# Kernel tuning notes

Measured on AMD Instinct MI355X. Metric: run time of the kernel, lower is better.

## Reference

```python
import jax, jax.numpy as jnp
import numpy as np

E, B, S, C, N, D, DFF, H, K_FREQ = 4, 16, 256, 17, 16, 32, 64, 4, 4
DH = D // H
MA_KERNELS = (4, 8, 12)


def setup_inputs() -> dict:
    key = jax.random.key(0)
    ks = jax.random.split(key, 16)
    sc = 1.0 / np.sqrt(D).astype(np.float32)
    inp = {
        "x": jax.random.normal(ks[0], (B, S, C, 1), jnp.float32),
        "original_x": jax.random.uniform(ks[1], (B, S, 2), jnp.float32),
        "start_W": jax.random.normal(ks[2], (D,), jnp.float32),
        "start_b": jnp.zeros((D,), jnp.float32),
        "Wq": jax.random.normal(ks[3], (E, D, D), jnp.float32) * sc,
        "Wk": jax.random.normal(ks[4], (E, D, D), jnp.float32) * sc,
        "Wv": jax.random.normal(ks[5], (E, D, D), jnp.float32) * sc,
        "Wo": jax.random.normal(ks[6], (E, D, D), jnp.float32) * sc,
        "ln1_g": jnp.ones((E, D), jnp.float32),
        "ln1_b": jnp.zeros((E, D), jnp.float32),
        "ln2_g": jnp.ones((E, D), jnp.float32),
        "ln2_b": jnp.zeros((E, D), jnp.float32),
        "W1": jax.random.normal(ks[7], (E, D, DFF), jnp.float32) * sc,
        "b1": jnp.zeros((E, DFF), jnp.float32),
        "W2": jax.random.normal(ks[8], (E, DFF, D), jnp.float32) * (1.0 / np.sqrt(DFF).astype(np.float32)),
        "b2": jnp.zeros((E, D), jnp.float32),
    }
    return inp


def _moving_avg(x, k):
    # x: [B,S,Ch], replicate-pad then uniform window of size k (stride 1)
    front = jnp.repeat(x[:, :1], (k - 1) // 2, axis=1)
    end = jnp.repeat(x[:, -1:], k // 2, axis=1)
    xp = jnp.concatenate([front, x, end], axis=1)  # [B, S+k-1, Ch]
    c = jnp.cumsum(xp, axis=1)
    c = jnp.concatenate([jnp.zeros_like(c[:, :1]), c], axis=1)
    return (c[:, k:] - c[:, :-k]) / jnp.asarray(k, x.dtype)


def _fourier_season(x, k):
    # ETSformer-style FourierLayer: keep top-k amplitude frequencies (excluding DC)
    s = x.shape[1]
    xf = jnp.fft.rfft(x, axis=1)            # [B,F,Ch] complex
    amp = jnp.abs(xf)
    amp = amp.at[:, 0, :].set(-jnp.inf)     # exclude DC
    topv = jax.lax.top_k(jnp.moveaxis(amp, 1, -1), k)[0]  # [B,Ch,k]
    thresh = topv[..., -1]                  # [B,Ch]
    mask = amp >= thresh[:, None, :]
    xf_m = jnp.where(mask, xf, 0)
    return jnp.fft.irfft(xf_m, n=s, axis=1).astype(x.dtype)


def _ln(z, g, b):
    m = jnp.mean(z, -1, keepdims=True)
    v = jnp.var(z, -1, keepdims=True)
    return (z - m) * jax.lax.rsqrt(v + 1e-5) * g + b


def _expert_fwd(args):
    h, wq, wk, wv, wo, g1, bg1, g2, bg2, w1, b1e, w2, b2e = args
    # h: [B,S,N,D]; pre-LN MHA over the sequence axis per (batch, node)
    z = _ln(h, g1, bg1)
    q = jnp.einsum('bsnd,de->bsne', z, wq).reshape(B, S, N, H, DH)
    k_ = jnp.einsum('bsnd,de->bsne', z, wk).reshape(B, S, N, H, DH)
    v_ = jnp.einsum('bsnd,de->bsne', z, wv).reshape(B, S, N, H, DH)
    att = jnp.einsum('bqnhd,bknhd->bnhqk', q, k_) * (1.0 / np.sqrt(DH).astype(np.float32))
    att = jax.nn.softmax(att, axis=-1)
    o = jnp.einsum('bnhqk,bknhd->bqnhd', att, v_).reshape(B, S, N, D)
    h = h + jnp.einsum('bsnd,de->bsne', o, wo)
    z2 = _ln(h, g2, bg2)
    f = jax.nn.relu(jnp.einsum('bsnd,df->bsnf', z2, w1) + b1e)
    h = h + jnp.einsum('bsnf,fd->bsnd', f, w2) + b2e
    return h


def reference(x, original_x, start_W, start_b, Wq, Wk, Wv, Wo,
              ln1_g, ln1_b, ln2_g, ln2_b, W1, b1, W2, b2):
    xc = x[:, :, :, 0]                                  # [B,S,C]
    trend = sum(_moving_avg(xc, k) for k in MA_KERNELS) / float(len(MA_KERNELS))
    season = _fourier_season(xc, K_FREQ)
    new_x = xc + season + trend                         # [B,S,C]

    scores = original_x[:, :, -1]                       # [B,S]
    bins = jnp.linspace(scores.min(), scores.max(), E + 1)
    assign = jnp.clip(jnp.searchsorted(bins, scores, side='right') - 1, 0, E - 1)  # [B,S] int

    xns = new_x[:, :, :-1]                              # [B,S,N] drop score channel
    onehot = (assign[None] == jnp.arange(E)[:, None, None])          # [E,B,S] bool
    expert_in = xns[None] * onehot[..., None].astype(xns.dtype)      # [E,B,S,N] dense zero-padded dispatch
    hidden = expert_in[..., None] * start_W + start_b                # [E,B,S,N,D] start_linear

    outs = jax.lax.map(_expert_fwd, (hidden, Wq, Wk, Wv, Wo,
                                     ln1_g, ln1_b, ln2_g, ln2_b, W1, b1, W2, b2))  # [E,B,S,N,D]
    combined = jnp.einsum('ebs,ebsnd->bsnd', onehot.astype(outs.dtype), outs)      # one-hot combine
    return combined
```

## Files before the change

kernel.cpp:

```cpp
#include <hip/hip_runtime.h>
#include <hip/hip_fp16.h>
#include <math.h>

#define BB 16
#define SS 256
#define CC 17
#define NCH 16
#define DD 32
#define DFFN 64
#define HH 4
#define DH 8
#define EE 4

#define WS_K0 16
#define WS_V0 144
#define WS_XNS 512
#define WS_SPI (WS_XNS + BB*SS*NCH)
#define WS_WT  (WS_SPI + BB*SS + 64)

#define PRE 0.51006977f

typedef __fp16 hv2 __attribute__((ext_vector_type(2)));

__device__ __forceinline__ unsigned pkh2(float a, float b) {
  hv2 r = __builtin_amdgcn_cvt_pkrtz(a, b);
  unsigned u; __builtin_memcpy(&u, &r, 4);
  return u;
}
__device__ __forceinline__ float fd2(unsigned a, unsigned b, float c) {
  hv2 av, bv;
  __builtin_memcpy(&av, &a, 4);
  __builtin_memcpy(&bv, &b, 4);
  return __builtin_amdgcn_fdot2(av, bv, c, false);
}
__device__ __forceinline__ __half2 u2h2(unsigned u) {
  __half2 h; __builtin_memcpy(&h, &u, 4); return h;
}
template<int PAT>
__device__ __forceinline__ unsigned qdpp(unsigned v) {
  return (unsigned)__builtin_amdgcn_mov_dpp((int)v, PAT, 0xF, 0xF, true);
}
template<int PAT>
__device__ __forceinline__ float qdppf(float v) {
  return __uint_as_float(qdpp<PAT>(__float_as_uint(v)));
}

__launch_bounds__(1024)
__global__ void decomp_prep_kernel(const float* __restrict__ x,
                                   const float* __restrict__ ox,
                                   const float* __restrict__ sW,
                                   const float* __restrict__ sb,
                                   const float* __restrict__ g1,
                                   const float* __restrict__ bb1,
                                   const float* __restrict__ Wq,
                                   const float* __restrict__ Wk,
                                   const float* __restrict__ Wv,
                                   const float* __restrict__ Wo,
                                   const float* __restrict__ W1,
                                   const float* __restrict__ W2,
                                   float* __restrict__ ws) {
  const int t = threadIdx.x;
  if (blockIdx.x < 256) {
    const int b = blockIdx.x / NCH;
    const int c = blockIdx.x % NCH;
    __shared__ float xs[SS];
    __shared__ float prr[1024], pii[1024];
    __shared__ float amp[129];
    __shared__ float2 YY[129];
    __shared__ float sth;
    if (t < SS) xs[t] = x[(b*SS + t)*CC + c];
    __syncthreads();
    const float TH0 = 0.024543692606170259f;
    {
      const int f = (t & 127) + 1;
      const int chunk = t >> 7;
      const int s0 = chunk * 32;
      const int ph0 = (f * s0) & 255;
      float si, cr; sincosf(TH0*(float)ph0, &si, &cr);
      float s1, c1; sincosf(TH0*(float)f, &s1, &c1);
      float xr = 0.f, xi = 0.f;
      #pragma unroll 4
      for (int k = 0; k < 32; ++k) {
        float xvv = xs[s0 + k];
        xr += xvv * cr;
        xi -= xvv * si;
        float nc = cr*c1 - si*s1;
        si = si*c1 + cr*s1;
        cr = nc;
      }
// ... 153 lines not shown
          val = pkh2(src[ip*128], src[ip*128 + 64]);
        } else {
          int r = u - 6144;
          int a = r >> 11, rr = r & 2047;
          int row = rr >> 4, ip = rr & 15;
          int e = row >> 5, qq = row & 31;
          int d = (qq & 3)*8 + (qq >> 2);
          int jp = a*16 + ip;
          const float* src = W2 + e*2048 + d;
          val = pkh2(src[2*jp*32], src[(2*jp+1)*32]);
        }
        img[u] = val;
      }
    }
  } else {
    __shared__ float s_a[DD], s_c[DD];
    if (t < DD) { s_a[t] = sW[t]; s_c[t] = sb[t]; }
    __syncthreads();
    if (t == 0) {
      float mW = 0.f, mb = 0.f;
      for (int d = 0; d < DD; ++d) { mW += s_a[d]; mb += s_c[d]; }
      mW *= (1.0f/DD); mb *= (1.0f/DD);
      float A = 0.f, Bv = 0.f, Cv = 0.f;
      for (int d = 0; d < DD; ++d) {
        float a = s_a[d] - mW, c = s_c[d] - mb;
        s_a[d] = a; s_c[d] = c;
        A += a*a; Bv += a*c; Cv += c*c;
      }
      ws[8]  = A  * (1.0f/DD);
      ws[9]  = Bv * (1.0f/DD);
      ws[10] = Cv * (1.0f/DD);
    }
    __syncthreads();
    if (t < 384) {
      const int m = t >> 7, r = t & 127, e = r >> 5, j = r & 31;
      const float* Wm = (m == 0) ? Wq : (m == 1) ? Wk : Wv;
      float pp = 0.f, qq = 0.f, rr = 0.f;
      for (int d = 0; d < DD; ++d) {
        float w  = Wm[e*DD*DD + d*DD + j];
        float gg = g1[e*DD + d];
        pp += s_a[d]*gg*w;
        qq += s_c[d]*gg*w;
        rr += bb1[e*DD + d]*w;
      }
      float* pqr = ws + WS_WT + 10240;
      const int base = (m*EE + e)*96 + j;
      pqr[base]      = pp;
      pqr[base + 32] = qq;
      pqr[base + 64] = rr;
    }
  }
}

__launch_bounds__(1024, 4)
__global__ void fused_kernel(const float* __restrict__ ws,
    const float* __restrict__ g1, const float* __restrict__ bb1,
    const float* __restrict__ sW, const float* __restrict__ sb,
    const float* __restrict__ g2, const float* __restrict__ bb2,
    const float* __restrict__ b1, const float* __restrict__ b2,
    float* __restrict__ out) {
  const int blk = blockIdx.x;
  const int n = blk & 15;
  const int b = blk >> 4;
  const int t = threadIdx.x;
  const int p = t >> 2;
  const int hh = t & 3;
  __shared__ unsigned lds[20480];
  unsigned* wl = lds + 8192;

  {
    const unsigned* img = (const unsigned*)ws + WS_WT;
    const int wv = t >> 6;
    const int ln = t & 63;
    #pragma unroll
    for (int i = 0; i < 3; ++i) {
      const int ch = wv*3 + i;
      __builtin_amdgcn_global_load_lds(
          (const __attribute__((address_space(1))) unsigned*)(img + ch*256 + ln*4),
          (__attribute__((address_space(3))) unsigned*)(wl + ch*256 + ln*4),
          16, 0, 0);
    }
  }

  const int* SP  = (const int*)ws + WS_SPI;
  const int* OFF = SP + BB*SS;
  const int o1 = OFF[b*4+1], o2v = OFF[b*4+2], o3 = OFF[b*4+3];
  const int e = (p >= o1) + (p >= o2v) + (p >= o3);
  const int beg = (e==0) ? 0  : ((e==1) ? o1 : ((e==2) ? o2v : o3));
  const int end = (e==0) ? o1 : ((e==1) ? o2v : ((e==2) ? o3 : SS));
  const int s = SP[b*SS + p];
  const float xv = ws[WS_XNS + (b*SS + s)*NCH + n];

  const float Ac = ws[8], Bc = ws[9], Cc = ws[10];
  const float var = fmaf(xv, fmaf(Ac, xv, Bc + Bc), Cc);
  const float rs = rsqrtf(var + 1e-5f);
  const float alpha = rs * xv, beta = rs;
  __syncthreads();

  const float* pqr = (const float*)(wl + 10240);
  float q[DH], kk[DH], vv[DH];
  #pragma unroll
  for (int m = 0; m < 3; ++m) {
    const float* bp = &pqr[(m*EE + e)*96 + hh*DH];
    const float4 P0 = *(const float4*)(bp);
    const float4 P1 = *(const float4*)(bp + 4);
    const float4 Q0 = *(const float4*)(bp + 32);
    const float4 Q1 = *(const float4*)(bp + 36);
    const float4 R0 = *(const float4*)(bp + 64);
    const float4 R1 = *(const float4*)(bp + 68);
    float* dst = (m == 0) ? q : (m == 1) ? kk : vv;
    dst[0] = fmaf(alpha, P0.x, fmaf(beta, Q0.x, R0.x));
    dst[1] = fmaf(alpha, P0.y, fmaf(beta, Q0.y, R0.y));
    dst[2] = fmaf(alpha, P0.z, fmaf(beta, Q0.z, R0.z));
    dst[3] = fmaf(alpha, P0.w, fmaf(beta, Q0.w, R0.w));
    dst[4] = fmaf(alpha, P1.x, fmaf(beta, Q1.x, R1.x));
    dst[5] = fmaf(alpha, P1.y, fmaf(beta, Q1.y, R1.y));
    dst[6] = fmaf(alpha, P1.z, fmaf(beta, Q1.z, R1.z));
    dst[7] = fmaf(alpha, P1.w, fmaf(beta, Q1.w, R1.w));
  }
  #pragma unroll
  for (int dd = 0; dd < DH; ++dd) q[dd] *= PRE;

  *(uint4*)&lds[p*32 + hh*8]     = make_uint4(pkh2(kk[0],kk[1]), pkh2(kk[2],kk[3]),
                                              pkh2(kk[4],kk[5]), pkh2(kk[6],kk[7]));
  *(uint4*)&lds[p*32 + hh*8 + 4] = make_uint4(pkh2(vv[0],vv[1]), pkh2(vv[2],vv[3]),
                                              pkh2(vv[4],vv[5]), pkh2(vv[6],vv[7]));
  unsigned qp2[4];
  #pragma unroll
  for (int i = 0; i < 4; ++i) qp2[i] = pkh2(q[2*i], q[2*i+1]);
  float s0 = 0.f;
  #pragma unroll
  for (int d = 0; d < DH; ++d) s0 += q[d] * ws[WS_K0 + e*DD + hh*DH + d];
  __syncthreads();

  float wsum = 0.f;
  __half2 o2[4];
  #pragma unroll
  for (int i = 0; i < 4; ++i) o2[i] = u2h2(0u);
  int jk = beg;
  for (; jk + 1 < end; jk += 2) {
    uint4 ku0 = *(const uint4*)&lds[jk*32 + hh*8];
    uint4 vu0 = *(const uint4*)&lds[jk*32 + hh*8 + 4];
    uint4 ku1 = *(const uint4*)&lds[(jk+1)*32 + hh*8];
    uint4 vu1 = *(const uint4*)&lds[(jk+1)*32 + hh*8 + 4];
    float a0 = 0.f, a1 = 0.f;
    a0 = fd2(qp2[0], ku0.x, a0); a0 = fd2(qp2[1], ku0.y, a0);
    a0 = fd2(qp2[2], ku0.z, a0); a0 = fd2(qp2[3], ku0.w, a0);
    a1 = fd2(qp2[0], ku1.x, a1); a1 = fd2(qp2[1], ku1.y, a1);
    a1 = fd2(qp2[2], ku1.z, a1); a1 = fd2(qp2[3], ku1.w, a1);
    float w0f = __builtin_amdgcn_exp2f(a0);
    float w1f = __builtin_amdgcn_exp2f(a1);
    wsum += w0f + w1f;
    __half2 w20 = u2h2(pkh2(w0f, w0f));
    __half2 w21 = u2h2(pkh2(w1f, w1f));
    o2[0] = __hfma2(w20, u2h2(vu0.x), o2[0]);
    o2[1] = __hfma2(w20, u2h2(vu0.y), o2[1]);
    o2[2] = __hfma2(w20, u2h2(vu0.z), o2[2]);
    o2[3] = __hfma2(w20, u2h2(vu0.w), o2[3]);
    o2[0] = __hfma2(w21, u2h2(vu1.x), o2[0]);
    o2[1] = __hfma2(w21, u2h2(vu1.y), o2[1]);
    o2[2] = __hfma2(w21, u2h2(vu1.z), o2[2]);
    o2[3] = __hfma2(w21, u2h2(vu1.w), o2[3]);
  }
  if (jk < end) {
    uint4 ku = *(const uint4*)&lds[jk*32 + hh*8];
    uint4 vu = *(const uint4*)&lds[jk*32 + hh*8 + 4];
    float a = 0.f;
    a = fd2(qp2[0], ku.x, a); a = fd2(qp2[1], ku.y, a);
    a = fd2(qp2[2], ku.z, a); a = fd2(qp2[3], ku.w, a);
    float wf = __builtin_amdgcn_exp2f(a);
    wsum += wf;
    __half2 w2 = u2h2(pkh2(wf, wf));
    o2[0] = __hfma2(w2, u2h2(vu.x), o2[0]);
    o2[1] = __hfma2(w2, u2h2(vu.y), o2[1]);
    o2[2] = __hfma2(w2, u2h2(vu.z), o2[2]);
    o2[3] = __hfma2(w2, u2h2(vu.w), o2[3]);
  }
  float o[DH];
  #pragma unroll
  for (int i = 0; i < 4; ++i) {
    o[2*i]   = __low2float(o2[i]);
    o[2*i+1] = __high2float(o2[i]);
  }
  const int nmis = SS - (end - beg);
  float w0 = (float)nmis * __builtin_amdgcn_exp2f(s0);
  wsum += w0;
  #pragma unroll
  for (int d = 0; d < DH; ++d) o[d] += w0 * ws[WS_V0 + e*DD + hh*DH + d];
  float inv = 1.0f / wsum;
  #pragma unroll
  for (int d = 0; d < DH; ++d) o[d] *= inv;

  unsigned oq[4];
  #pragma unroll
  for (int j = 0; j < 4; ++j) oq[j] = pkh2(o[2*j], o[2*j+1]);
  unsigned ovp[16];
  #pragma unroll
  for (int j = 0; j < 4; ++j) {
    ovp[j]    = qdpp<0x00>(oq[j]);
    ovp[4+j]  = qdpp<0x55>(oq[j]);
    ovp[8+j]  = qdpp<0xAA>(oq[j]);
    ovp[12+j] = qdpp<0xFF>(oq[j]);
  }

  float acc[DH];
  #pragma unroll
  for (int dd = 0; dd < DH; ++dd) {
    int d = hh*DH + dd;
    const uint4* row = (const uint4*)&wl[(e*32 + dd*4 + hh)*16];
    float a = xv * sW[d] + sb[d];
    #pragma unroll
    for (int g4 = 0; g4 < 4; ++g4) {
      uint4 w4 = row[g4];
      a = fd2(ovp[4*g4+0], w4.x, a); a = fd2(ovp[4*g4+1], w4.y, a);
      a = fd2(ovp[4*g4+2], w4.z, a); a = fd2(ovp[4*g4+3], w4.w, a);
    }
    acc[dd] = a;
  }

  float ssum = 0.f;
  #pragma unroll
  for (int dd = 0; dd < DH; ++dd) ssum += acc[dd];
  ssum += qdppf<0xB1>(ssum);
  ssum += qdppf<0x4E>(ssum);
  float m2 = ssum * (1.0f/DD);
  float vs = 0.f;
  #pragma unroll
  for (int dd = 0; dd < DH; ++dd) { float df = acc[dd]-m2; vs += df*df; }
  vs += qdppf<0xB1>(vs);
  vs += qdppf<0x4E>(vs);
  float rs2 = rsqrtf(vs * (1.0f/DD) + 1e-5f);
  unsigned zq[4];
  #pragma unroll
  for (int j = 0; j < 4; ++j) {
    int d = hh*DH + 2*j;
    float za = (acc[2*j]  -m2)*rs2*g2[e*DD+d]   + bb2[e*DD+d];
    float zb = (acc[2*j+1]-m2)*rs2*g2[e*DD+d+1] + bb2[e*DD+d+1];
    zq[j] = pkh2(za, zb);
  }
  unsigned zp2[16];
  #pragma unroll
  for (int j = 0; j < 4; ++j) {
    zp2[j]    = qdpp<0x00>(zq[j]);
    zp2[4+j]  = qdpp<0x55>(zq[j]);
    zp2[8+j]  = qdpp<0xAA>(zq[j]);
    zp2[12+j] = qdpp<0xFF>(zq[j]);
  }

  float f[16];
  #pragma unroll
  for (int jj = 0; jj < 16; ++jj) {
    const uint4* row = (const uint4*)&wl[2048 + (e*64 + jj*4 + hh)*16];
    float a = b1[e*DFFN + hh*16 + jj];
    #pragma unroll
    for (int g4 = 0; g4 < 4; ++g4) {
      uint4 w4 = row[g4];
      a = fd2(zp2[4*g4+0], w4.x, a); a = fd2(zp2[4*g4+1], w4.y, a);
      a = fd2(zp2[4*g4+2], w4.z, a); a = fd2(zp2[4*g4+3], w4.w, a);
    }
    f[jj] = fmaxf(a, 0.0f);
  }
  unsigned fq[8];
  #pragma unroll
  for (int j = 0; j < 8; ++j) fq[j] = pkh2(f[2*j], f[2*j+1]);
  unsigned fu[32];
  #pragma unroll
  for (int j = 0; j < 8; ++j) {
    fu[j]    = qdpp<0x00>(fq[j]);
    fu[8+j]  = qdpp<0x55>(fq[j]);
    fu[16+j] = qdpp<0xAA>(fq[j]);
    fu[24+j] = qdpp<0xFF>(fq[j]);
  }

  float acc2[DH];
  #pragma unroll
  for (int dd = 0; dd < DH; ++dd) {
    int d = hh*DH + dd;
    const int row16 = (e*32 + dd*4 + hh)*16;
    float a = acc[dd] + b2[e*DD + d];
    #pragma unroll
    for (int g4 = 0; g4 < 8; ++g4) {
      const int plane = (g4 >> 2);
      uint4 w4 = *(const uint4*)&wl[6144 + plane*2048 + row16 + 4*(g4 & 3)];
      a = fd2(fu[4*g4+0], w4.x, a); a = fd2(fu[4*g4+1], w4.y, a);
      a = fd2(fu[4*g4+2], w4.z, a); a = fd2(fu[4*g4+3], w4.w, a);
    }
    acc2[dd] = a;
  }
  float* op = out + ((size_t)((b*SS + s)*NCH + n))*DD + hh*DH;
  *(float4*)(op)     = make_float4(acc2[0], acc2[1], acc2[2], acc2[3]);
  *(float4*)(op + 4) = make_float4(acc2[4], acc2[5], acc2[6], acc2[7]);
}

extern "C" void kernel_launch(void* const* d_in, const int* in_sizes, int n_in,
                              void* d_out, int out_size, void* d_ws, size_t ws_size,
                              hipStream_t stream) {
  (void)in_sizes; (void)n_in; (void)out_size; (void)ws_size;
  const float* x   = (const float*)d_in[0];
  const float* ox  = (const float*)d_in[1];
  const float* sW  = (const float*)d_in[2];
  const float* sb  = (const float*)d_in[3];
  const float* Wq  = (const float*)d_in[4];
  const float* Wk  = (const float*)d_in[5];
  const float* Wv  = (const float*)d_in[6];
  const float* Wo  = (const float*)d_in[7];
  const float* g1  = (const float*)d_in[8];
  const float* b1n = (const float*)d_in[9];
  const float* g2  = (const float*)d_in[10];
  const float* b2n = (const float*)d_in[11];
  const float* W1  = (const float*)d_in[12];
  const float* bf1 = (const float*)d_in[13];
  const float* W2  = (const float*)d_in[14];
  const float* bf2 = (const float*)d_in[15];
  float* out = (float*)d_out;
  float* ws  = (float*)d_ws;

  decomp_prep_kernel<<<276, 1024, 0, stream>>>(x, ox, sW, sb, g1, b1n,
                                               Wq, Wk, Wv, Wo, W1, W2, ws);
  fused_kernel<<<BB*NCH, 1024, 0, stream>>>(ws, g1, b1n, sW, sb, g2, b2n,
                                            bf1, bf2, out);
}
```

Measured before the change: 135.6 us.

## Process two positions per thread to reuse K/V and weight LDS loads

```diff
diff --git a/kernel.cpp b/kernel.cpp
--- a/kernel.cpp
+++ b/kernel.cpp
@@ -294,7 +294,121 @@
   }
 }
 
-__launch_bounds__(1024, 4)
+template<int NP>
+__device__ __forceinline__ void post_attn(
+    const unsigned* wl, int e, int hh,
+    const float* sW, const float* sb,
+    const float* g2, const float* bb2,
+    const float* b1, const float* b2,
+    const float* xv,
+    const unsigned (*oq)[4],
+    float* const* op) {
+  float acc[NP][DH];
+  #pragma unroll
+  for (int u = 0; u < NP; ++u)
+    #pragma unroll
+    for (int dd = 0; dd < DH; ++dd) {
+      const int d = hh*DH + dd;
+      acc[u][dd] = xv[u]*sW[d] + sb[d];
+    }
+
+#define WO_G(PAT, G) { \
+    unsigned ol[NP][4]; \
+    _Pragma("unroll") for (int u = 0; u < NP; ++u) { \
+      ol[u][0]=qdpp<PAT>(oq[u][0]); ol[u][1]=qdpp<PAT>(oq[u][1]); \
+      ol[u][2]=qdpp<PAT>(oq[u][2]); ol[u][3]=qdpp<PAT>(oq[u][3]); } \
+    _Pragma("unroll") for (int dd = 0; dd < DH; ++dd) { \
+      const uint4 w4 = *(const uint4*)&wl[(e*32 + dd*4 + hh)*16 + 4*(G)]; \
+      _Pragma("unroll") for (int u = 0; u < NP; ++u) { \
+        float a = acc[u][dd]; \
+        a = fd2(ol[u][0], w4.x, a); a = fd2(ol[u][1], w4.y, a); \
+        a = fd2(ol[u][2], w4.z, a); a = fd2(ol[u][3], w4.w, a); \
+        acc[u][dd] = a; } } }
+  WO_G(0x00, 0) WO_G(0x55, 1) WO_G(0xAA, 2) WO_G(0xFF, 3)
+#undef WO_G
+
+  unsigned zq[NP][4];
+  #pragma unroll
+  for (int u = 0; u < NP; ++u) {
+    float ssum = 0.f;
+    #pragma unroll
+    for (int dd = 0; dd < DH; ++dd) ssum += acc[u][dd];
+    ssum += qdppf<0xB1>(ssum);
+    ssum += qdppf<0x4E>(ssum);
+    const float m2 = ssum * (1.0f/DD);
+    float vs = 0.f;
+    #pragma unroll
+    for (int dd = 0; dd < DH; ++dd) { float df = acc[u][dd]-m2; vs += df*df; }
+    vs += qdppf<0xB1>(vs);
+    vs += qdppf<0x4E>(vs);
+    const float rs2 = rsqrtf(vs * (1.0f/DD) + 1e-5f);
+    #pragma unroll
+    for (int j = 0; j < 4; ++j) {
+      const int d = hh*DH + 2*j;
+      float za = (acc[u][2*j]  -m2)*rs2*g2[e*DD+d]   + bb2[e*DD+d];
+      float zb = (acc[u][2*j+1]-m2)*rs2*g2[e*DD+d+1] + bb2[e*DD+d+1];
+      zq[u][j] = pkh2(za, zb);
+    }
+  }
+
+  float f[NP][16];
+  #pragma unroll
+  for (int u = 0; u < NP; ++u)
+    #pragma unroll
+    for (int jj = 0; jj < 16; ++jj) f[u][jj] = b1[e*DFFN + hh*16 + jj];
+#define F1_G(PAT, G) { \
+    unsigned zl[NP][4]; \
+    _Pragma("unroll") for (int u = 0; u < NP; ++u) { \
+      zl[u][0]=qdpp<PAT>(zq[u][0]); zl[u][1]=qdpp<PAT>(zq[u][1]); \
+      zl[u][2]=qdpp<PAT>(zq[u][2]); zl[u][3]=qdpp<PAT>(zq[u][3]); } \
+    _Pragma("unroll") for (int jj = 0; jj < 16; ++jj) { \
+      const uint4 w4 = *(const uint4*)&wl[2048 + (e*64 + jj*4 + hh)*16 + 4*(G)]; \
+      _Pragma("unroll") for (int u = 0; u < NP; ++u) { \
+        float a = f[u][jj]; \
+        a = fd2(zl[u][0], w4.x, a); a = fd2(zl[u][1], w4.y, a); \
+        a = fd2(zl[u][2], w4.z, a); a = fd2(zl[u][3], w4.w, a); \
+        f[u][jj] = a; } } }
+  F1_G(0x00, 0) F1_G(0x55, 1) F1_G(0xAA, 2) F1_G(0xFF, 3)
+#undef F1_G
+  unsigned fq[NP][8];
+  #pragma unroll
+  for (int u = 0; u < NP; ++u)
+    #pragma unroll
+    for (int j = 0; j < 8; ++j)
+      fq[u][j] = pkh2(fmaxf(f[u][2*j], 0.0f), fmaxf(f[u][2*j+1], 0.0f));
+
+  float acc2[NP][DH];
+  #pragma unroll
+  for (int u = 0; u < NP; ++u)
+    #pragma unroll
+    for (int dd = 0; dd < DH; ++dd)
+      acc2[u][dd] = acc[u][dd] + b2[e*DD + hh*DH + dd];
+#define F2_L(PAT, L) { \
+    unsigned fl[NP][8]; \
+    _Pragma("unroll") for (int u = 0; u < NP; ++u) \
+      _Pragma("unroll") for (int j = 0; j < 8; ++j) fl[u][j] = qdpp<PAT>(fq[u][j]); \
+    _Pragma("unroll") for (int dd = 0; dd < DH; ++dd) { \
+      const int row16 = (e*32 + dd*4 + hh)*16; \
+      const uint4 wA = *(const uint4*)&wl[6144 + ((L)>>1)*2048 + row16 + 4*((2*(L))&3)]; \
+      const uint4 wB = *(const uint4*)&wl[6144 + ((L)>>1)*2048 + row16 + 4*((2*(L)+1)&3)]; \
+      _Pragma("unroll") for (int u = 0; u < NP; ++u) { \
+        float a = acc2[u][dd]; \
+        a = fd2(fl[u][0], wA.x, a); a = fd2(fl[u][1], wA.y, a); \
+        a = fd2(fl[u][2], wA.z, a); a = fd2(fl[u][3], wA.w, a); \
+        a = fd2(fl[u][4], wB.x, a); a = fd2(fl[u][5], wB.y, a); \
+        a = fd2(fl[u][6], wB.z, a); a = fd2(fl[u][7], wB.w, a); \
+        acc2[u][dd] = a; } } }
+  F2_L(0x00, 0) F2_L(0x55, 1) F2_L(0xAA, 2) F2_L(0xFF, 3)
+#undef F2_L
+
+  #pragma unroll
+  for (int u = 0; u < NP; ++u) {
+    *(float4*)(op[u])     = make_float4(acc2[u][0], acc2[u][1], acc2[u][2], acc2[u][3]);
+    *(float4*)(op[u] + 4) = make_float4(acc2[u][4], acc2[u][5], acc2[u][6], acc2[u][7]);
+  }
+}
+
+__launch_bounds__(512, 2)
 __global__ void fused_kernel(const float* __restrict__ ws,
     const float* __restrict__ g1, const float* __restrict__ bb1,
     const float* __restrict__ sW, const float* __restrict__ sb,
@@ -305,9 +419,10 @@
   const int n = blk & 15;
   const int b = blk >> 4;
   const int t = threadIdx.x;
-  const int p = t >> 2;
+  const int pr = t >> 2;
   const int hh = t & 3;
-  __shared__ unsigned lds[20480];
+  const int p0 = pr*2, p1 = pr*2 + 1;
+  __shared__ unsigned lds[18432];
   unsigned* wl = lds + 8192;
 
   {
@@ -315,8 +430,8 @@
     const int wv = t >> 6;
     const int ln = t & 63;
     #pragma unroll
-    for (int i = 0; i < 3; ++i) {
-      const int ch = wv*3 + i;
+    for (int i = 0; i < 5; ++i) {
+      const int ch = wv*5 + i;
       __builtin_amdgcn_global_load_lds(
           (const __attribute__((address_space(1))) unsigned*)(img + ch*256 + ln*4),
           (__attribute__((address_space(3))) unsigned*)(wl + ch*256 + ln*4),
@@ -327,211 +442,223 @@
   const int* SP  = (const int*)ws + WS_SPI;
   const int* OFF = SP + BB*SS;
   const int o1 = OFF[b*4+1], o2v = OFF[b*4+2], o3 = OFF[b*4+3];
-  const int e = (p >= o1) + (p >= o2v) + (p >= o3);
-  const int beg = (e==0) ? 0  : ((e==1) ? o1 : ((e==2) ? o2v : o3));
-  const int end = (e==0) ? o1 : ((e==1) ? o2v : ((e==2) ? o3 : SS));
-  const int s = SP[b*SS + p];
-  const float xv = ws[WS_XNS + (b*SS + s)*NCH + n];
+  const int e0 = (p0 >= o1) + (p0 >= o2v) + (p0 >= o3);
+  const int e1 = (p1 >= o1) + (p1 >= o2v) + (p1 >= o3);
+  const int beg0 = (e0==0) ? 0  : ((e0==1) ? o1 : ((e0==2) ? o2v : o3));
+  const int end0 = (e0==0) ? o1 : ((e0==1) ? o2v : ((e0==2) ? o3 : SS));
+  const int beg1 = (e1==0) ? 0  : ((e1==1) ? o1 : ((e1==2) ? o2v : o3));
+  const int end1 = (e1==0) ? o1 : ((e1==1) ? o2v : ((e1==2) ? o3 : SS));
+  const int s_0 = SP[b*SS + p0];
+  const int s_1 = SP[b*SS + p1];
+  const float xv0 = ws[WS_XNS + (b*SS + s_0)*NCH + n];
+  const float xv1 = ws[WS_XNS + (b*SS + s_1)*NCH + n];
 
   const float Ac = ws[8], Bc = ws[9], Cc = ws[10];
-  const float var = fmaf(xv, fmaf(Ac, xv, Bc + Bc), Cc);
-  const float rs = rsqrtf(var + 1e-5f);
-  const float alpha = rs * xv, beta = rs;
+  const float rs0 = rsqrtf(fmaf(xv0, fmaf(Ac, xv0, Bc + Bc), Cc) + 1e-5f);
+  const float rs1 = rsqrtf(fmaf(xv1, fmaf(Ac, xv1, Bc + Bc), Cc) + 1e-5f);
+  const float al0 = rs0*xv0, be0 = rs0;
+  const float al1 = rs1*xv1, be1 = rs1;
+
+  const float* pqr = ws + WS_WT + 10240;
+  float q0[DH], ka0[DH], va0[DH], q1[DH], ka1[DH], va1[DH];
+  {
+    #pragma unroll
+    for (int m = 0; m < 3; ++m) {
+      {
+        const float* bp = &pqr[(m*EE + e0)*96 + hh*DH];
+        const float4 P0 = *(const float4*)(bp),    P1 = *(const float4*)(bp + 4);
+        const float4 Q0 = *(const float4*)(bp+32), Q1 = *(const float4*)(bp + 36);
+        const float4 R0 = *(const float4*)(bp+64), R1 = *(const float4*)(bp + 68);
+        float* dst = (m == 0) ? q0 : (m == 1) ? ka0 : va0;
+        dst[0] = fmaf(al0, P0.x, fmaf(be0, Q0.x, R0.x));
+        dst[1] = fmaf(al0, P0.y, fmaf(be0, Q0.y, R0.y));
+        dst[2] = fmaf(al0, P0.z, fmaf(be0, Q0.z, R0.z));
+        dst[3] = fmaf(al0, P0.w, fmaf(be0, Q0.w, R0.w));
+        dst[4] = fmaf(al0, P1.x, fmaf(be0, Q1.x, R1.x));
+        dst[5] = fmaf(al0, P1.y, fmaf(be0, Q1.y, R1.y));
+        dst[6] = fmaf(al0, P1.z, fmaf(be0, Q1.z, R1.z));
+        dst[7] = fmaf(al0, P1.w, fmaf(be0, Q1.w, R1.w));
+      }
+      {
+        const float* bp = &pqr[(m*EE + e1)*96 + hh*DH];
+        const float4 P0 = *(const float4*)(bp),    P1 = *(const float4*)(bp + 4);
+        const float4 Q0 = *(const float4*)(bp+32), Q1 = *(const float4*)(bp + 36);
+        const float4 R0 = *(const float4*)(bp+64), R1 = *(const float4*)(bp + 68);
+        float* dst = (m == 0) ? q1 : (m == 1) ? ka1 : va1;
+        dst[0] = fmaf(al1, P0.x, fmaf(be1, Q0.x, R0.x));
+        dst[1] = fmaf(al1, P0.y, fmaf(be1, Q0.y, R0.y));
+        dst[2] = fmaf(al1, P0.z, fmaf(be1, Q0.z, R0.z));
+        dst[3] = fmaf(al1, P0.w, fmaf(be1, Q0.w, R0.w));
+        dst[4] = fmaf(al1, P1.x, fmaf(be1, Q1.x, R1.x));
+        dst[5] = fmaf(al1, P1.y, fmaf(be1, Q1.y, R1.y));
+        dst[6] = fmaf(al1, P1.z, fmaf(be1, Q1.z, R1.z));
+        dst[7] = fmaf(al1, P1.w, fmaf(be1, Q1.w, R1.w));
+      }
+    }
+  }
+  #pragma unroll
+  for (int d = 0; d < DH; ++d) { q0[d] *= PRE; q1[d] *= PRE; }
+
+  *(uint4*)&lds[p0*32 + hh*8]     = make_uint4(pkh2(ka0[0],ka0[1]), pkh2(ka0[2],ka0[3]),
+                                               pkh2(ka0[4],ka0[5]), pkh2(ka0[6],ka0[7]));
+  *(uint4*)&lds[p0*32 + hh*8 + 4] = make_uint4(pkh2(va0[0],va0[1]), pkh2(va0[2],va0[3]),
+                                               pkh2(va0[4],va0[5]), pkh2(va0[6],va0[7]));
+  *(uint4*)&lds[p1*32 + hh*8]     = make_uint4(pkh2(ka1[0],ka1[1]), pkh2(ka1[2],ka1[3]),
+                                               pkh2(ka1[4],ka1[5]), pkh2(ka1[6],ka1[7]));
+  *(uint4*)&lds[p1*32 + hh*8 + 4] = make_uint4(pkh2(va1[0],va1[1]), pkh2(va1[2],va1[3]),
+                                               pkh2(va1[4],va1[5]), pkh2(va1[6],va1[7]));
+  unsigned qp0[4], qp1[4];
+  #pragma unroll
+  for (int i = 0; i < 4; ++i) {
+    qp0[i] = pkh2(q0[2*i], q0[2*i+1]);
+    qp1[i] = pkh2(q1[2*i], q1[2*i+1]);
+  }
+  float s0_0 = 0.f, s0_1 = 0.f;
+  {
+    const float4 Ka = *(const float4*)&ws[WS_K0 + e0*DD + hh*DH];
+    const float4 Kb = *(const float4*)&ws[WS_K0 + e0*DD + hh*DH + 4];
+    s0_0 = q0[0]*Ka.x + q0[1]*Ka.y + q0[2]*Ka.z + q0[3]*Ka.w
+         + q0[4]*Kb.x + q0[5]*Kb.y + q0[6]*Kb.z + q0[7]*Kb.w;
+    const float4 Kc = *(const float4*)&ws[WS_K0 + e1*DD + hh*DH];
+    const float4 Kd = *(const float4*)&ws[WS_K0 + e1*DD + hh*DH + 4];
+    s0_1 = q1[0]*Kc.x + q1[1]*Kc.y + q1[2]*Kc.z + q1[3]*Kc.w
+         + q1[4]*Kd.x + q1[5]*Kd.y + q1[6]*Kd.z + q1[7]*Kd.w;
+  }
   __syncthreads();
 
-  const float* pqr = (const float*)(wl + 10240);
-  float q[DH], kk[DH], vv[DH];
-  #pragma unroll
-  for (int m = 0; m < 3; ++m) {
-    const float* bp = &pqr[(m*EE + e)*96 + hh*DH];
-    const float4 P0 = *(const float4*)(bp);
-    const float4 P1 = *(const float4*)(bp + 4);
-    const float4 Q0 = *(const float4*)(bp + 32);
-    const float4 Q1 = *(const float4*)(bp + 36);
-    const float4 R0 = *(const float4*)(bp + 64);
-    const float4 R1 = *(const float4*)(bp + 68);
-    float* dst = (m == 0) ? q : (m == 1) ? kk : vv;
-    dst[0] = fmaf(alpha, P0.x, fmaf(beta, Q0.x, R0.x));
-    dst[1] = fmaf(alpha, P0.y, fmaf(beta, Q0.y, R0.y));
-    dst[2] = fmaf(alpha, P0.z, fmaf(beta, Q0.z, R0.z));
-    dst[3] = fmaf(alpha, P0.w, fmaf(beta, Q0.w, R0.w));
-    dst[4] = fmaf(alpha, P1.x, fmaf(beta, Q1.x, R1.x));
-    dst[5] = fmaf(alpha, P1.y, fmaf(beta, Q1.y, R1.y));
-    dst[6] = fmaf(alpha, P1.z, fmaf(beta, Q1.z, R1.z));
-    dst[7] = fmaf(alpha, P1.w, fmaf(beta, Q1.w, R1.w));
-  }
-  #pragma unroll
-  for (int dd = 0; dd < DH; ++dd) q[dd] *= PRE;
-
-  *(uint4*)&lds[p*32 + hh*8]     = make_uint4(pkh2(kk[0],kk[1]), pkh2(kk[2],kk[3]),
-                                              pkh2(kk[4],kk[5]), pkh2(kk[6],kk[7]));
-  *(uint4*)&lds[p*32 + hh*8 + 4] = make_uint4(pkh2(vv[0],vv[1]), pkh2(vv[2],vv[3]),
-                                              pkh2(vv[4],vv[5]), pkh2(vv[6],vv[7]));
-  unsigned qp2[4];
-  #pragma unroll
-  for (int i = 0; i < 4; ++i) qp2[i] = pkh2(q[2*i], q[2*i+1]);
-  float s0 = 0.f;
-  #pragma unroll
-  for (int d = 0; d < DH; ++d) s0 += q[d] * ws[WS_K0 + e*DD + hh*DH + d];
-  __syncthreads();
-
-  float wsum = 0.f;
-  __half2 o2[4];
-  #pragma unroll
-  for (int i = 0; i < 4; ++i) o2[i] = u2h2(0u);
-  int jk = beg;
-  for (; jk + 1 < end; jk += 2) {
-    uint4 ku0 = *(const uint4*)&lds[jk*32 + hh*8];
-    uint4 vu0 = *(const uint4*)&lds[jk*32 + hh*8 + 4];
-    uint4 ku1 = *(const uint4*)&lds[(jk+1)*32 + hh*8];
-    uint4 vu1 = *(const uint4*)&lds[(jk+1)*32 + hh*8 + 4];
+  float ws0 = 0.f, ws1 = 0.f;
+  __half2 oa0[4], oa1[4];
+  #pragma unroll
+  for (int i = 0; i < 4; ++i) { oa0[i] = u2h2(0u); oa1[i] = u2h2(0u); }
+  int jk = beg0;
+  for (; jk + 1 < end1; jk += 2) {
+    const uint4 kua = *(const uint4*)&lds[jk*32 + hh*8];
+    const uint4 vua = *(const uint4*)&lds[jk*32 + hh*8 + 4];
+    const uint4 kub = *(const uint4*)&lds[(jk+1)*32 + hh*8];
+    const uint4 vub = *(const uint4*)&lds[(jk+1)*32 + hh*8 + 4];
+    float a0a = 0.f, a1a = 0.f, a0b = 0.f, a1b = 0.f;
+    a0a = fd2(qp0[0], kua.x, a0a); a0a = fd2(qp0[1], kua.y, a0a);
+    a0a = fd2(qp0[2], kua.z, a0a); a0a = fd2(qp0[3], kua.w, a0a);
+    a1a = fd2(qp1[0], kua.x, a1a); a1a = fd2(qp1[1], kua.y, a1a);
+    a1a = fd2(qp1[2], kua.z, a1a); a1a = fd2(qp1[3], kua.w, a1a);
+    a0b = fd2(qp0[0], kub.x, a0b); a0b = fd2(qp0[1], kub.y, a0b);
+    a0b = fd2(qp0[2], kub.z, a0b); a0b = fd2(qp0[3], kub.w, a0b);
+    a1b = fd2(qp1[0], kub.x, a1b); a1b = fd2(qp1[1], kub.y, a1b);
+    a1b = fd2(qp1[2], kub.z, a1b); a1b = fd2(qp1[3], kub.w, a1b);
+    const float w0a = (jk   < end0) ? __builtin_amdgcn_exp2f(a0a) : 0.f;
+    const float w1a = (jk   >= beg1) ? __builtin_amdgcn_exp2f(a1a) : 0.f;
+    const float w0b = (jk+1 < end0) ? __builtin_amdgcn_exp2f(a0b) : 0.f;
+    const float w1b = (jk+1 >= beg1) ? __builtin_amdgcn_exp2f(a1b) : 0.f;
+    ws0 += w0a + w0b;
+    ws1 += w1a + w1b;
+    const __half2 h0a = u2h2(pkh2(w0a, w0a));
+    const __half2 h1a = u2h2(pkh2(w1a, w1a));
+    const __half2 h0b = u2h2(pkh2(w0b, w0b));
+    const __half2 h1b = u2h2(pkh2(w1b, w1b));
+    oa0[0] = __hfma2(h0a, u2h2(vua.x), oa0[0]);
+    oa0[1] = __hfma2(h0a, u2h2(vua.y), oa0[1]);
+    oa0[2] = __hfma2(h0a, u2h2(vua.z), oa0[2]);
+    oa0[3] = __hfma2(h0a, u2h2(vua.w), oa0[3]);
+    oa1[0] = __hfma2(h1a, u2h2(vua.x), oa1[0]);
+    oa1[1] = __hfma2(h1a, u2h2(vua.y), oa1[1]);
+    oa1[2] = __hfma2(h1a, u2h2(vua.z), oa1[2]);
+    oa1[3] = __hfma2(h1a, u2h2(vua.w), oa1[3]);
+    oa0[0] = __hfma2(h0b, u2h2(vub.x), oa0[0]);
+    oa0[1] = __hfma2(h0b, u2h2(vub.y), oa0[1]);
+    oa0[2] = __hfma2(h0b, u2h2(vub.z), oa0[2]);
+    oa0[3] = __hfma2(h0b, u2h2(vub.w), oa0[3]);
+    oa1[0] = __hfma2(h1b, u2h2(vub.x), oa1[0]);
+    oa1[1] = __hfma2(h1b, u2h2(vub.y), oa1[1]);
+    oa1[2] = __hfma2(h1b, u2h2(vub.z), oa1[2]);
+    oa1[3] = __hfma2(h1b, u2h2(vub.w), oa1[3]);
+  }
+  if (jk < end1) {
+    const uint4 ku = *(const uint4*)&lds[jk*32 + hh*8];
+    const uint4 vu = *(const uint4*)&lds[jk*32 + hh*8 + 4];
     float a0 = 0.f, a1 = 0.f;
-    a0 = fd2(qp2[0], ku0.x, a0); a0 = fd2(qp2[1], ku0.y, a0);
-    a0 = fd2(qp2[2], ku0.z, a0); a0 = fd2(qp2[3], ku0.w, a0);
-    a1 = fd2(qp2[0], ku1.x, a1); a1 = fd2(qp2[1], ku1.y, a1);
-    a1 = fd2(qp2[2], ku1.z, a1); a1 = fd2(qp2[3], ku1.w, a1);
-    float w0f = __builtin_amdgcn_exp2f(a0);
-    float w1f = __builtin_amdgcn_exp2f(a1);
-    wsum += w0f + w1f;
-    __half2 w20 = u2h2(pkh2(w0f, w0f));
-    __half2 w21 = u2h2(pkh2(w1f, w1f));
-    o2[0] = __hfma2(w20, u2h2(vu0.x), o2[0]);
-    o2[1] = __hfma2(w20, u2h2(vu0.y), o2[1]);
-    o2[2] = __hfma2(w20, u2h2(vu0.z), o2[2]);
-    o2[3] = __hfma2(w20, u2h2(vu0.w), o2[3]);
-    o2[0] = __hfma2(w21, u2h2(vu1.x), o2[0]);
-    o2[1] = __hfma2(w21, u2h2(vu1.y), o2[1]);
-    o2[2] = __hfma2(w21, u2h2(vu1.z), o2[2]);
-    o2[3] = __hfma2(w21, u2h2(vu1.w), o2[3]);
-  }
-  if (jk < end) {
-    uint4 ku = *(const uint4*)&lds[jk*32 + hh*8];
-    uint4 vu = *(const uint4*)&lds[jk*32 + hh*8 + 4];
-    float a = 0.f;
-    a = fd2(qp2[0], ku.x, a); a = fd2(qp2[1], ku.y, a);
-    a = fd2(qp2[2], ku.z, a); a = fd2(qp2[3], ku.w, a);
-    float wf = __builtin_amdgcn_exp2f(a);
-    wsum += wf;
-    __half2 w2 = u2h2(pkh2(wf, wf));
-    o2[0] = __hfma2(w2, u2h2(vu.x), o2[0]);
-    o2[1] = __hfma2(w2, u2h2(vu.y), o2[1]);
-    o2[2] = __hfma2(w2, u2h2(vu.z), o2[2]);
-    o2[3] = __hfma2(w2, u2h2(vu.w), o2[3]);
-  }
-  float o[DH];
-  #pragma unroll
-  for (int i = 0; i < 4; ++i) {
-    o[2*i]   = __low2float(o2[i]);
-    o[2*i+1] = __high2float(o2[i]);
-  }
-  const int nmis = SS - (end - beg);
-  float w0 = (float)nmis * __builtin_amdgcn_exp2f(s0);
-  wsum += w0;
-  #pragma unroll
-  for (int d = 0; d < DH; ++d) o[d] += w0 * ws[WS_V0 + e*DD + hh*DH + d];
-  float inv = 1.0f / wsum;
-  #pragma unroll
-  for (int d = 0; d < DH; ++d) o[d] *= inv;
-
-  unsigned oq[4];
-  #pragma unroll
-  for (int j = 0; j < 4; ++j) oq[j] = pkh2(o[2*j], o[2*j+1]);
-  unsigned ovp[16];
-  #pragma unroll
-  for (int j = 0; j < 4; ++j) {
-    ovp[j]    = qdpp<0x00>(oq[j]);
-    ovp[4+j]  = qdpp<0x55>(oq[j]);
-    ovp[8+j]  = qdpp<0xAA>(oq[j]);
-    ovp[12+j] = qdpp<0xFF>(oq[j]);
-  }
-
-  float acc[DH];
-  #pragma unroll
-  for (int dd = 0; dd < DH; ++dd) {
-    int d = hh*DH + dd;
-    const uint4* row = (const uint4*)&wl[(e*32 + dd*4 + hh)*16];
-    float a = xv * sW[d] + sb[d];
-    #pragma unroll
-    for (int g4 = 0; g4 < 4; ++g4) {
-      uint4 w4 = row[g4];
-      a = fd2(ovp[4*g4+0], w4.x, a); a = fd2(ovp[4*g4+1], w4.y, a);
-      a = fd2(ovp[4*g4+2], w4.z, a); a = fd2(ovp[4*g4+3], w4.w, a);
-    }
-    acc[dd] = a;
-  }
-
-  float ssum = 0.f;
-  #pragma unroll
-  for (int dd = 0; dd < DH; ++dd) ssum += acc[dd];
-  ssum += qdppf<0xB1>(ssum);
-  ssum += qdppf<0x4E>(ssum);
-  float m2 = ssum * (1.0f/DD);
-  float vs = 0.f;
-  #pragma unroll
-  for (int dd = 0; dd < DH; ++dd) { float df = acc[dd]-m2; vs += df*df; }
-  vs += qdppf<0xB1>(vs);
-  vs += qdppf<0x4E>(vs);
-  float rs2 = rsqrtf(vs * (1.0f/DD) + 1e-5f);
-  unsigned zq[4];
-  #pragma unroll
-  for (int j = 0; j < 4; ++j) {
-    int d = hh*DH + 2*j;
-    float za = (acc[2*j]  -m2)*rs2*g2[e*DD+d]   + bb2[e*DD+d];
-    float zb = (acc[2*j+1]-m2)*rs2*g2[e*DD+d+1] + bb2[e*DD+d+1];
-    zq[j] = pkh2(za, zb);
-  }
-  unsigned zp2[16];
-  #pragma unroll
-  for (int j = 0; j < 4; ++j) {
-    zp2[j]    = qdpp<0x00>(zq[j]);
-    zp2[4+j]  = qdpp<0x55>(zq[j]);
-    zp2[8+j]  = qdpp<0xAA>(zq[j]);
-    zp2[12+j] = qdpp<0xFF>(zq[j]);
-  }
-
-  float f[16];
-  #pragma unroll
-  for (int jj = 0; jj < 16; ++jj) {
-    const uint4* row = (const uint4*)&wl[2048 + (e*64 + jj*4 + hh)*16];
-    float a = b1[e*DFFN + hh*16 + jj];
-    #pragma unroll
-    for (int g4 = 0; g4 < 4; ++g4) {
-      uint4 w4 = row[g4];
-      a = fd2(zp2[4*g4+0], w4.x, a); a = fd2(zp2[4*g4+1], w4.y, a);
-      a = fd2(zp2[4*g4+2], w4.z, a); a = fd2(zp2[4*g4+3], w4.w, a);
-    }
-    f[jj] = fmaxf(a, 0.0f);
-  }
-  unsigned fq[8];
-  #pragma unroll
-  for (int j = 0; j < 8; ++j) fq[j] = pkh2(f[2*j], f[2*j+1]);
-  unsigned fu[32];
-  #pragma unroll
-  for (int j = 0; j < 8; ++j) {
-    fu[j]    = qdpp<0x00>(fq[j]);
-    fu[8+j]  = qdpp<0x55>(fq[j]);
-    fu[16+j] = qdpp<0xAA>(fq[j]);
-    fu[24+j] = qdpp<0xFF>(fq[j]);
-  }
-
-  float acc2[DH];
-  #pragma unroll
-  for (int dd = 0; dd < DH; ++dd) {
-    int d = hh*DH + dd;
-    const int row16 = (e*32 + dd*4 + hh)*16;
-    float a = acc[dd] + b2[e*DD + d];
-    #pragma unroll
-    for (int g4 = 0; g4 < 8; ++g4) {
-      const int plane = (g4 >> 2);
-      uint4 w4 = *(const uint4*)&wl[6144 + plane*2048 + row16 + 4*(g4 & 3)];
-      a = fd2(fu[4*g4+0], w4.x, a); a = fd2(fu[4*g4+1], w4.y, a);
-      a = fd2(fu[4*g4+2], w4.z, a); a = fd2(fu[4*g4+3], w4.w, a);
-    }
-    acc2[dd] = a;
-  }
-  float* op = out + ((size_t)((b*SS + s)*NCH + n))*DD + hh*DH;
-  *(float4*)(op)     = make_float4(acc2[0], acc2[1], acc2[2], acc2[3]);
-  *(float4*)(op + 4) = make_float4(acc2[4], acc2[5], acc2[6], acc2[7]);
+    a0 = fd2(qp0[0], ku.x, a0); a0 = fd2(qp0[1], ku.y, a0);
+    a0 = fd2(qp0[2], ku.z, a0); a0 = fd2(qp0[3], ku.w, a0);
+    a1 = fd2(qp1[0], ku.x, a1); a1 = fd2(qp1[1], ku.y, a1);
+    a1 = fd2(qp1[2], ku.z, a1); a1 = fd2(qp1[3], ku.w, a1);
+    const float w0 = (jk < end0)  ? __builtin_amdgcn_exp2f(a0) : 0.f;
+    const float w1 = (jk >= beg1) ? __builtin_amdgcn_exp2f(a1) : 0.f;
+    ws0 += w0; ws1 += w1;
+    const __half2 h0 = u2h2(pkh2(w0, w0));
+    const __half2 h1 = u2h2(pkh2(w1, w1));
+    oa0[0] = __hfma2(h0, u2h2(vu.x), oa0[0]);
+    oa0[1] = __hfma2(h0, u2h2(vu.y), oa0[1]);
+    oa0[2] = __hfma2(h0, u2h2(vu.z), oa0[2]);
+    oa0[3] = __hfma2(h0, u2h2(vu.w), oa0[3]);
+    oa1[0] = __hfma2(h1, u2h2(vu.x), oa1[0]);
+    oa1[1] = __hfma2(h1, u2h2(vu.y), oa1[1]);
+    oa1[2] = __hfma2(h1, u2h2(vu.z), oa1[2]);
+    oa1[3] = __hfma2(h1, u2h2(vu.w), oa1[3]);
+  }
+
+  unsigned oq0[4], oq1[4];
+  {
+    float o[DH];
+    #pragma unroll
+    for (int i = 0; i < 4; ++i) { o[2*i] = __low2float(oa0[i]); o[2*i+1] = __high2float(oa0[i]); }
+    const int nmis = SS - (end0 - beg0);
+    const float w0c = (float)nmis * __builtin_amdgcn_exp2f(s0_0);
+    float wsum = ws0 + w0c;
+    const float4 Va = *(const float4*)&ws[WS_V0 + e0*DD + hh*DH];
+    const float4 Vb = *(const float4*)&ws[WS_V0 + e0*DD + hh*DH + 4];
+    o[0] += w0c*Va.x; o[1] += w0c*Va.y; o[2] += w0c*Va.z; o[3] += w0c*Va.w;
+    o[4] += w0c*Vb.x; o[5] += w0c*Vb.y; o[6] += w0c*Vb.z; o[7] += w0c*Vb.w;
+    const float inv = 1.0f / wsum;
+    #pragma unroll
+    for (int d = 0; d < DH; ++d) o[d] *= inv;
+    #pragma unroll
+    for (int j = 0; j < 4; ++j) oq0[j] = pkh2(o[2*j], o[2*j+1]);
+  }
+  {
+    float o[DH];
+    #pragma unroll
+    for (int i = 0; i < 4; ++i) { o[2*i] = __low2float(oa1[i]); o[2*i+1] = __high2float(oa1[i]); }
+    const int nmis = SS - (end1 - beg1);
+    const float w0c = (float)nmis * __builtin_amdgcn_exp2f(s0_1);
+    float wsum = ws1 + w0c;
+    const float4 Va = *(const float4*)&ws[WS_V0 + e1*DD + hh*DH];
+    const float4 Vb = *(const float4*)&ws[WS_V0 + e1*DD + hh*DH + 4];
+    o[0] += w0c*Va.x; o[1] += w0c*Va.y; o[2] += w0c*Va.z; o[3] += w0c*Va.w;
+    o[4] += w0c*Vb.x; o[5] += w0c*Vb.y; o[6] += w0c*Vb.z; o[7] += w0c*Vb.w;
+    const float inv = 1.0f / wsum;
+    #pragma unroll
+    for (int d = 0; d < DH; ++d) o[d] *= inv;
+    #pragma unroll
+    for (int j = 0; j < 4; ++j) oq1[j] = pkh2(o[2*j], o[2*j+1]);
+  }
+
+  float* op0 = out + ((size_t)((b*SS + s_0)*NCH + n))*DD + hh*DH;
+  float* op1 = out + ((size_t)((b*SS + s_1)*NCH + n))*DD + hh*DH;
+
+  if (e0 == e1) {
+    const float xvv[2] = {xv0, xv1};
+    unsigned oqq[2][4];
+    #pragma unroll
+    for (int j = 0; j < 4; ++j) { oqq[0][j] = oq0[j]; oqq[1][j] = oq1[j]; }
+    float* opp[2] = {op0, op1};
+    post_attn<2>(wl, e0, hh, sW, sb, g2, bb2, b1, b2, xvv, oqq, opp);
+  } else {
+    {
+      const float xvv[1] = {xv0};
+      unsigned oqq[1][4];
+      #pragma unroll
+      for (int j = 0; j < 4; ++j) oqq[0][j] = oq0[j];
+      float* opp[1] = {op0};
+      post_attn<1>(wl, e0, hh, sW, sb, g2, bb2, b1, b2, xvv, oqq, opp);
+    }
+    {
+      const float xvv[1] = {xv1};
+      unsigned oqq[1][4];
+      #pragma unroll
+      for (int j = 0; j < 4; ++j) oqq[0][j] = oq1[j];
+      float* opp[1] = {op1};
+      post_attn<1>(wl, e1, hh, sW, sb, g2, bb2, b1, b2, xvv, oqq, opp);
+    }
+  }
 }
 
 extern "C" void kernel_launch(void* const* d_in, const int* in_sizes, int n_in,
@@ -559,6 +686,6 @@
 
   decomp_prep_kernel<<<276, 1024, 0, stream>>>(x, ox, sW, sb, g1, b1n,
                                                Wq, Wk, Wv, Wo, W1, W2, ws);
-  fused_kernel<<<BB*NCH, 1024, 0, stream>>>(ws, g1, b1n, sW, sb, g2, b2n,
-                                            bf1, bf2, out);
-}
+  fused_kernel<<<BB*NCH, 512, 0, stream>>>(ws, g1, b1n, sW, sb, g2, b2n,
+                                           bf1, bf2, out);
+}
```

Measured after the change: 152.7 us. +12.7%, slower.

## Split key range between sibling query pairs and share K/V loads across them

Applied to the files above, without the earlier changes.

```diff
diff --git a/kernel.cpp b/kernel.cpp
--- a/kernel.cpp
+++ b/kernel.cpp
@@ -35,6 +35,12 @@
 }
 __device__ __forceinline__ __half2 u2h2(unsigned u) {
   __half2 h; __builtin_memcpy(&h, &u, 4); return h;
+}
+__device__ __forceinline__ __half2 shx_h2(__half2 x, int m) {
+  int v; __builtin_memcpy(&v, &x, 4);
+  v = __shfl_xor(v, m);
+  __half2 r; __builtin_memcpy(&r, &v, 4);
+  return r;
 }
 template<int PAT>
 __device__ __forceinline__ unsigned qdpp(unsigned v) {
@@ -305,8 +311,10 @@
   const int n = blk & 15;
   const int b = blk >> 4;
   const int t = threadIdx.x;
-  const int p = t >> 2;
   const int hh = t & 3;
+  const int sk = (t >> 2) & 1;
+  const int p  = (t >> 3)*2 + sk;
+  const int psib = p ^ 1;
   __shared__ unsigned lds[20480];
   unsigned* wl = lds + 8192;
 
@@ -330,6 +338,9 @@
   const int e = (p >= o1) + (p >= o2v) + (p >= o3);
   const int beg = (e==0) ? 0  : ((e==1) ? o1 : ((e==2) ? o2v : o3));
   const int end = (e==0) ? o1 : ((e==1) ? o2v : ((e==2) ? o3 : SS));
+  const int es = (psib >= o1) + (psib >= o2v) + (psib >= o3);
+  const int begs = (es==0) ? 0  : ((es==1) ? o1 : ((es==2) ? o2v : o3));
+  const int ends = (es==0) ? o1 : ((es==1) ? o2v : ((es==2) ? o3 : SS));
   const int s = SP[b*SS + p];
   const float xv = ws[WS_XNS + (b*SS + s)*NCH + n];
 
@@ -367,57 +378,91 @@
                                               pkh2(kk[4],kk[5]), pkh2(kk[6],kk[7]));
   *(uint4*)&lds[p*32 + hh*8 + 4] = make_uint4(pkh2(vv[0],vv[1]), pkh2(vv[2],vv[3]),
                                               pkh2(vv[4],vv[5]), pkh2(vv[6],vv[7]));
-  unsigned qp2[4];
+  unsigned qp2[4], qsb[4];
   #pragma unroll
   for (int i = 0; i < 4; ++i) qp2[i] = pkh2(q[2*i], q[2*i+1]);
+  #pragma unroll
+  for (int i = 0; i < 4; ++i) qsb[i] = (unsigned)__shfl_xor((int)qp2[i], 4);
   float s0 = 0.f;
   #pragma unroll
   for (int d = 0; d < DH; ++d) s0 += q[d] * ws[WS_K0 + e*DD + hh*DH + d];
   __syncthreads();
 
-  float wsum = 0.f;
+  const int lo = (beg < begs) ? beg : begs;
+  const int hi = (end > ends) ? end : ends;
+  float wsO = 0.f, wsS = 0.f;
+  __half2 oaO[4], oaS[4];
+  #pragma unroll
+  for (int i = 0; i < 4; ++i) { oaO[i] = u2h2(0u); oaS[i] = u2h2(0u); }
+  int jk = lo + sk;
+  for (; jk + 2 < hi; jk += 4) {
+    const uint4 ku0 = *(const uint4*)&lds[jk*32 + hh*8];
+    const uint4 vu0 = *(const uint4*)&lds[jk*32 + hh*8 + 4];
+    const uint4 ku1 = *(const uint4*)&lds[(jk+2)*32 + hh*8];
+    const uint4 vu1 = *(const uint4*)&lds[(jk+2)*32 + hh*8 + 4];
+    float aO0 = 0.f, aS0 = 0.f, aO1 = 0.f, aS1 = 0.f;
+    aO0 = fd2(qp2[0], ku0.x, aO0); aO0 = fd2(qp2[1], ku0.y, aO0);
+    aO0 = fd2(qp2[2], ku0.z, aO0); aO0 = fd2(qp2[3], ku0.w, aO0);
+    aS0 = fd2(qsb[0], ku0.x, aS0); aS0 = fd2(qsb[1], ku0.y, aS0);
+    aS0 = fd2(qsb[2], ku0.z, aS0); aS0 = fd2(qsb[3], ku0.w, aS0);
+    aO1 = fd2(qp2[0], ku1.x, aO1); aO1 = fd2(qp2[1], ku1.y, aO1);
+    aO1 = fd2(qp2[2], ku1.z, aO1); aO1 = fd2(qp2[3], ku1.w, aO1);
+    aS1 = fd2(qsb[0], ku1.x, aS1); aS1 = fd2(qsb[1], ku1.y, aS1);
+    aS1 = fd2(qsb[2], ku1.z, aS1); aS1 = fd2(qsb[3], ku1.w, aS1);
+    const float wO0 = (jk   >= beg  && jk   < end)  ? __builtin_amdgcn_exp2f(aO0) : 0.f;
+    const float wS0 = (jk   >= begs && jk   < ends) ? __builtin_amdgcn_exp2f(aS0) : 0.f;
+    const float wO1 = (jk+2 >= beg  && jk+2 < end)  ? __builtin_amdgcn_exp2f(aO1) : 0.f;
+    const float wS1 = (jk+2 >= begs && jk+2 < ends) ? __builtin_amdgcn_exp2f(aS1) : 0.f;
+    wsO += wO0 + wO1;
+    wsS += wS0 + wS1;
+    const __half2 hO0 = u2h2(pkh2(wO0, wO0));
+    const __half2 hS0 = u2h2(pkh2(wS0, wS0));
+    const __half2 hO1 = u2h2(pkh2(wO1, wO1));
+    const __half2 hS1 = u2h2(pkh2(wS1, wS1));
+    oaO[0] = __hfma2(hO0, u2h2(vu0.x), oaO[0]);
+    oaO[1] = __hfma2(hO0, u2h2(vu0.y), oaO[1]);
+    oaO[2] = __hfma2(hO0, u2h2(vu0.z), oaO[2]);
+    oaO[3] = __hfma2(hO0, u2h2(vu0.w), oaO[3]);
+    oaS[0] = __hfma2(hS0, u2h2(vu0.x), oaS[0]);
+    oaS[1] = __hfma2(hS0, u2h2(vu0.y), oaS[1]);
+    oaS[2] = __hfma2(hS0, u2h2(vu0.z), oaS[2]);
+    oaS[3] = __hfma2(hS0, u2h2(vu0.w), oaS[3]);
+    oaO[0] = __hfma2(hO1, u2h2(vu1.x), oaO[0]);
+    oaO[1] = __hfma2(hO1, u2h2(vu1.y), oaO[1]);
+    oaO[2] = __hfma2(hO1, u2h2(vu1.z), oaO[2]);
+    oaO[3] = __hfma2(hO1, u2h2(vu1.w), oaO[3]);
+    oaS[0] = __hfma2(hS1, u2h2(vu1.x), oaS[0]);
+    oaS[1] = __hfma2(hS1, u2h2(vu1.y), oaS[1]);
+    oaS[2] = __hfma2(hS1, u2h2(vu1.z), oaS[2]);
+    oaS[3] = __hfma2(hS1, u2h2(vu1.w), oaS[3]);
+  }
+  if (jk < hi) {
+    const uint4 ku = *(const uint4*)&lds[jk*32 + hh*8];
+    const uint4 vu = *(const uint4*)&lds[jk*32 + hh*8 + 4];
+    float aO = 0.f, aS = 0.f;
+    aO = fd2(qp2[0], ku.x, aO); aO = fd2(qp2[1], ku.y, aO);
+    aO = fd2(qp2[2], ku.z, aO); aO = fd2(qp2[3], ku.w, aO);
+    aS = fd2(qsb[0], ku.x, aS); aS = fd2(qsb[1], ku.y, aS);
+    aS = fd2(qsb[2], ku.z, aS); aS = fd2(qsb[3], ku.w, aS);
+    const float wO = (jk >= beg  && jk < end)  ? __builtin_amdgcn_exp2f(aO) : 0.f;
+    const float wS = (jk >= begs && jk < ends) ? __builtin_amdgcn_exp2f(aS) : 0.f;
+    wsO += wO; wsS += wS;
+    const __half2 hO = u2h2(pkh2(wO, wO));
+    const __half2 hS = u2h2(pkh2(wS, wS));
+    oaO[0] = __hfma2(hO, u2h2(vu.x), oaO[0]);
+    oaO[1] = __hfma2(hO, u2h2(vu.y), oaO[1]);
+    oaO[2] = __hfma2(hO, u2h2(vu.z), oaO[2]);
+    oaO[3] = __hfma2(hO, u2h2(vu.w), oaO[3]);
+    oaS[0] = __hfma2(hS, u2h2(vu.x), oaS[0]);
+    oaS[1] = __hfma2(hS, u2h2(vu.y), oaS[1]);
+    oaS[2] = __hfma2(hS, u2h2(vu.z), oaS[2]);
+    oaS[3] = __hfma2(hS, u2h2(vu.w), oaS[3]);
+  }
+  float wsum = wsO + __shfl_xor(wsS, 4);
   __half2 o2[4];
   #pragma unroll
-  for (int i = 0; i < 4; ++i) o2[i] = u2h2(0u);
-  int jk = beg;
-  for (; jk + 1 < end; jk += 2) {
-    uint4 ku0 = *(const uint4*)&lds[jk*32 + hh*8];
-    uint4 vu0 = *(const uint4*)&lds[jk*32 + hh*8 + 4];
-    uint4 ku1 = *(const uint4*)&lds[(jk+1)*32 + hh*8];
-    uint4 vu1 = *(const uint4*)&lds[(jk+1)*32 + hh*8 + 4];
-    float a0 = 0.f, a1 = 0.f;
-    a0 = fd2(qp2[0], ku0.x, a0); a0 = fd2(qp2[1], ku0.y, a0);
-    a0 = fd2(qp2[2], ku0.z, a0); a0 = fd2(qp2[3], ku0.w, a0);
-    a1 = fd2(qp2[0], ku1.x, a1); a1 = fd2(qp2[1], ku1.y, a1);
-    a1 = fd2(qp2[2], ku1.z, a1); a1 = fd2(qp2[3], ku1.w, a1);
-    float w0f = __builtin_amdgcn_exp2f(a0);
-    float w1f = __builtin_amdgcn_exp2f(a1);
-    wsum += w0f + w1f;
-    __half2 w20 = u2h2(pkh2(w0f, w0f));
-    __half2 w21 = u2h2(pkh2(w1f, w1f));
-    o2[0] = __hfma2(w20, u2h2(vu0.x), o2[0]);
-    o2[1] = __hfma2(w20, u2h2(vu0.y), o2[1]);
-    o2[2] = __hfma2(w20, u2h2(vu0.z), o2[2]);
-    o2[3] = __hfma2(w20, u2h2(vu0.w), o2[3]);
-    o2[0] = __hfma2(w21, u2h2(vu1.x), o2[0]);
-    o2[1] = __hfma2(w21, u2h2(vu1.y), o2[1]);
-    o2[2] = __hfma2(w21, u2h2(vu1.z), o2[2]);
-    o2[3] = __hfma2(w21, u2h2(vu1.w), o2[3]);
-  }
-  if (jk < end) {
-    uint4 ku = *(const uint4*)&lds[jk*32 + hh*8];
-    uint4 vu = *(const uint4*)&lds[jk*32 + hh*8 + 4];
-    float a = 0.f;
-    a = fd2(qp2[0], ku.x, a); a = fd2(qp2[1], ku.y, a);
-    a = fd2(qp2[2], ku.z, a); a = fd2(qp2[3], ku.w, a);
-    float wf = __builtin_amdgcn_exp2f(a);
-    wsum += wf;
-    __half2 w2 = u2h2(pkh2(wf, wf));
-    o2[0] = __hfma2(w2, u2h2(vu.x), o2[0]);
-    o2[1] = __hfma2(w2, u2h2(vu.y), o2[1]);
-    o2[2] = __hfma2(w2, u2h2(vu.z), o2[2]);
-    o2[3] = __hfma2(w2, u2h2(vu.w), o2[3]);
-  }
+  for (int i = 0; i < 4; ++i) o2[i] = __hadd2(oaO[i], shx_h2(oaS[i], 4));
+
   float o[DH];
   #pragma unroll
   for (int i = 0; i < 4; ++i) {
```

New measurement: 138.4 us. 1.02x slower.
